# Optimization experiments

Hardware: AMD Instinct MI355X
Metric: run time of the kernel (lower is better)

## Reference

```python
import jax, jax.numpy as jnp
import numpy as np

N_NODES = 8192
GNN_DIM = 512
N_FEAT = 64
N_ITER = 4


def setup_inputs() -> dict:
    key = jax.random.key(0)
    ks = jax.random.split(key, 8)
    scale = 1.0 / np.sqrt(GNN_DIM)
    return {
        "labels": jax.random.normal(ks[0], (N_NODES, GNN_DIM), dtype=jnp.float32),
        "adj": jax.random.uniform(ks[1], (N_NODES, N_NODES), dtype=jnp.float32),
        "features": jax.random.normal(ks[2], (N_FEAT,), dtype=jnp.float32),
        "W_self": jax.random.normal(ks[3], (GNN_DIM, GNN_DIM), dtype=jnp.float32) * scale,
        "b_self": jax.random.normal(ks[4], (GNN_DIM,), dtype=jnp.float32) * scale,
        "W_neigh": jax.random.normal(ks[5], (GNN_DIM, GNN_DIM), dtype=jnp.float32) * scale,
        "W_fc": jax.random.normal(ks[6], (1, GNN_DIM + N_FEAT), dtype=jnp.float32) * scale,
        "b_fc": jax.random.normal(ks[7], (1,), dtype=jnp.float32) * scale,
    }


def reference(labels, adj, features, W_self, b_self, W_neigh, W_fc, b_fc):
    x = labels  # [N, D]
    for _ in range(N_ITER):
        acc = adj @ x                                   # [N, D] neighbor aggregation
        x = jax.nn.relu(x @ W_self.T + b_self + acc @ W_neigh.T)
    pooled = jnp.mean(x, axis=0)                        # [D]
    z = jnp.concatenate([pooled, features]) @ W_fc.T + b_fc  # [1]
    return jax.nn.sigmoid(z)
```

## Files before the change

### kernel.cpp

```cpp
#include <hip/hip_runtime.h>

typedef __bf16 bf16;
typedef bf16 bf16x8 __attribute__((ext_vector_type(8)));
typedef bf16 bf16x4 __attribute__((ext_vector_type(4)));
typedef float f32x4 __attribute__((ext_vector_type(4)));
typedef long longx2 __attribute__((ext_vector_type(2)));
typedef unsigned int u32;
typedef unsigned int u32x2 __attribute__((ext_vector_type(2)));
typedef unsigned int u32x4 __attribute__((ext_vector_type(4)));
typedef unsigned char u8;
typedef unsigned long long u64;

constexpr int NN = 8192;
constexpr int DD = 512;
constexpr size_t PSZB = (size_t)NN * DD * 2;
constexpr size_t PSZE = (size_t)NN * DD;
constexpr int NS = 4;

static __device__ inline bf16x8 cvt8(const float* __restrict__ p) {
  f32x4 a = *(const f32x4*)p;
  f32x4 b = *(const f32x4*)(p + 4);
  bf16x8 r;
  r[0] = (bf16)a[0]; r[1] = (bf16)a[1]; r[2] = (bf16)a[2]; r[3] = (bf16)a[3];
  r[4] = (bf16)b[0]; r[5] = (bf16)b[1]; r[6] = (bf16)b[2]; r[7] = (bf16)b[3];
  return r;
}

static __device__ inline unsigned f32_to_e4m3(float x) {
  float a = fabsf(x);
  unsigned s = (__float_as_uint(x) >> 24) & 0x80u;
  if (!(a < 448.f)) a = 448.f;
  if (a < 0.015625f)
    return s | (unsigned)(int)__builtin_rintf(a * 512.f);
  int e = (int)((__float_as_uint(a) >> 23) & 0xFF) - 127;
  float mul = __uint_as_float((unsigned)(130 - e) << 23);
  int t = (int)__builtin_rintf(a * mul);
  return s | (unsigned)((e + 6) * 8 + t);
}

#define GLDS(g, l) __builtin_amdgcn_global_load_lds( \
    (const __attribute__((address_space(1))) unsigned int*)(const void*)(g), \
    (__attribute__((address_space(3))) unsigned int*)(void*)(l), 16, 0, 0)


__global__ __launch_bounds__(256) void convert_w_kernel(
    const float* __restrict__ a, const float* __restrict__ b,
    bf16* __restrict__ ao, bf16* __restrict__ bo, float* __restrict__ pooled) {
  int tid = (int)threadIdx.x;
  if (blockIdx.x == 0) {
    pooled[tid] = 0.f;
    pooled[tid + 256] = 0.f;
  }
  int i8 = ((int)blockIdx.x * 256 + tid) * 8;
  if (i8 < DD * DD) {
    *(bf16x8*)&ao[i8] = cvt8(a + i8);
  } else {
    int j = i8 - DD * DD;
    *(bf16x8*)&bo[j] = cvt8(b + j);
  }
}

__global__ __launch_bounds__(256) void convert_adj_kernel(
    const float* __restrict__ a, u8* __restrict__ o) {
  int i = (int)blockIdx.x * 256 + (int)threadIdx.x;
  int row = i >> 9;
  int rem = i & 511;
  int g = rem >> 2, fq = rem & 3;
  const float* p = a + (size_t)row * NN + g * 64 + fq * 8;
  f32x4 v0 = *(const f32x4*)p;
  f32x4 v1 = *(const f32x4*)(p + 4);
  f32x4 v2 = *(const f32x4*)(p + 32);
  f32x4 v3 = *(const f32x4*)(p + 36);
  u32 w0 = 0, w1 = 0, w2 = 0, w3 = 0;
  w0 = __builtin_amdgcn_cvt_pk_fp8_f32(v0[0], v0[1], w0, false);
  w0 = __builtin_amdgcn_cvt_pk_fp8_f32(v0[2], v0[3], w0, true);
  w1 = __builtin_amdgcn_cvt_pk_fp8_f32(v1[0], v1[1], w1, false);
  w1 = __builtin_amdgcn_cvt_pk_fp8_f32(v1[2], v1[3], w1, true);
  w2 = __builtin_amdgcn_cvt_pk_fp8_f32(v2[0], v2[1], w2, false);
  w2 = __builtin_amdgcn_cvt_pk_fp8_f32(v2[2], v2[3], w2, true);
  w3 = __builtin_amdgcn_cvt_pk_fp8_f32(v3[0], v3[1], w3, false);
  w3 = __builtin_amdgcn_cvt_pk_fp8_f32(v3[2], v3[3], w3, true);
  u32x4 w; w[0] = w0; w[1] = w1; w[2] = w2; w[3] = w3;
  *(u32x4*)(o + (size_t)row * NN + g * 64 + fq * 16) = w;
}

__global__ __launch_bounds__(256) void convert_x_kernel(
    const float* __restrict__ src, bf16* __restrict__ xb, u8* __restrict__ xbT8) {
  __shared__ __align__(16) float tile[64][68];
  const int tid = (int)threadIdx.x;
  const int r0 = (int)blockIdx.x * 64;
  const int c0 = (int)blockIdx.y * 64;
#pragma unroll
  for (int p = 0; p < 4; ++p) {
    int row = p * 16 + (tid >> 4);
    int col = (tid & 15) * 4;
    *(f32x4*)&tile[row][col] = *(const f32x4*)&src[(size_t)(r0 + row) * DD + c0 + col];
  }
  __syncthreads();
#pragma unroll
  for (int p = 0; p < 4; ++p) {
    int row = p * 16 + (tid >> 4);
    int col = (tid & 15) * 4;
    f32x4 v = *(const f32x4*)&tile[row][col];
    bf16x4 o;
    o[0] = (bf16)v[0]; o[1] = (bf16)v[1]; o[2] = (bf16)v[2]; o[3] = (bf16)v[3];
    *(bf16x4*)&xb[(size_t)(r0 + row) * DD + c0 + col] = o;
  }
  {
    int c = tid >> 2;
    int rp = (tid & 3) * 16;
    size_t base = (size_t)(c0 + c) * NN + r0;
#pragma unroll
    for (int b = 0; b < 2; ++b) {
      u32 lo = 0, hi = 0;
      lo = __builtin_amdgcn_cvt_pk_fp8_f32(tile[rp + 8 * b + 0][c], tile[rp + 8 * b + 1][c], lo, false);
      lo = __builtin_amdgcn_cvt_pk_fp8_f32(tile[rp + 8 * b + 2][c], tile[rp + 8 * b + 3][c], lo, true);
      hi = __builtin_amdgcn_cvt_pk_fp8_f32(tile[rp + 8 * b + 4][c], tile[rp + 8 * b + 5][c], hi, false);
      hi = __builtin_amdgcn_cvt_pk_fp8_f32(tile[rp + 8 * b + 6][c], tile[rp + 8 * b + 7][c], hi, true);
      int u = (rp >> 3) + b;
      u32x2 w; w[0] = lo; w[1] = hi;
      *(u32x2*)&xbT8[base + (u & 3) * 16 + (u >> 2) * 8] = w;
    }
  }
}


__device__ __forceinline__ void stage_half8(const u8* __restrict__ g, int grow0, int k0b,
                                            u8* smbase, int wave, int lane) {
  int row = grow0 + wave * 16 + (lane >> 2);
  int col = k0b + (((lane & 3) ^ ((lane >> 2) & 3)) << 4);
  GLDS(g + (size_t)row * NN + col, smbase + wave * 1024);
}

__global__ __launch_bounds__(512, 2)
void gemm1_kernel(const u8* __restrict__ adjb, const u8* __restrict__ xbT8,
                  bf16* __restrict__ pbase) {
  __shared__ __align__(16) u8 sm[65536];
  const int bid  = (int)blockIdx.x;
  const int xcd  = bid & 7, ii = bid >> 3;
  const int cb   = ii & 1;
  const int jj_  = xcd + 8 * (ii >> 1);
  const int p    = jj_ >> 2;
  const int s    = jj_ & 3;
  const int prow0 = p * 256;
  const int bcol0 = cb * 256;
  const int kb    = s * 2048;
  bf16* __restrict__ P = pbase + (size_t)s * PSZE;

  const int tid  = (int)threadIdx.x;
  const int lane = tid & 63;
  const int wave = tid >> 6;
  const int wr   = wave >> 2;
  const int wc   = wave & 3;
  const int fr   = lane & 15, fq = lane >> 4;

  f32x4 acc[8][4] = {};

#define A_OFF(par) ((par) * 32768)
#define B_OFF(par) ((par) * 32768 + 16384)
#define STAGE_A(tile, half, par) \
  stage_half8(adjb, prow0 + (half) * 128, kb + ((tile) & 31) * 64, \
              sm + A_OFF(par) + (half) * 8192, wave, lane)
#define STAGE_B(tile, half, par) \
  stage_half8(xbT8, bcol0 + (half) * 128, kb + ((tile) & 31) * 64, \
              sm + B_OFF(par) + (half) * 8192, wave, lane)

  STAGE_B(0, 0, 0); STAGE_B(0, 1, 0); STAGE_A(0, 0, 0);
  STAGE_A(0, 1, 0); STAGE_B(1, 0, 1); STAGE_B(1, 1, 1); STAGE_A(1, 0, 1);

  longx2 bvp[4], afp[2];

#define LOAD_B(par)                                                        \
  _Pragma("unroll") for (int n = 0; n < 4; ++n) {                          \
    int rowl = wc * 64 + n * 16 + fr;                                      \
    int slot = fq ^ (rowl & 3);                                            \
    bvp[n] = *(const longx2*)&sm[B_OFF(par) + rowl * 64 + slot * 16];      \
  }
#define LOAD_A(q, par)                                                     \
  _Pragma("unroll") for (int j = 0; j < 2; ++j) {                          \
    int rowl = (q) * 64 + wr * 32 + j * 16 + fr;                           \
    int slot = fq ^ (rowl & 3);                                            \
    afp[j] = *(const longx2*)&sm[A_OFF(par) + rowl * 64 + slot * 16];      \
  }
#define QMFMA(q)                                                           \
  _Pragma("unroll") for (int kk = 0; kk < 2; ++kk)                         \
  _Pragma("unroll") for (int j = 0; j < 2; ++j)                            \
  _Pragma("unroll") for (int n = 0; n < 4; ++n)                            \
    acc[2 * (q) + j][n] = __builtin_amdgcn_mfma_f32_16x16x32_fp8_fp8(      \
        kk ? afp[j].y : afp[j].x, kk ? bvp[n].y : bvp[n].x,                \
        acc[2 * (q) + j][n], 0, 0, 0);
#define PHASE_TAIL(q)                                                      \
  __builtin_amdgcn_s_barrier();                                            \
  asm volatile("s_waitcnt lgkmcnt(0)" ::: "memory");                       \
  __builtin_amdgcn_sched_barrier(0);                                       \
  __builtin_amdgcn_s_setprio(1);                                           \
  QMFMA(q);                                                                \
  __builtin_amdgcn_s_setprio(0);                                           \
  __builtin_amdgcn_s_barrier();

  for (int it = 0; it < 16; ++it) {
    const int t = it * 2;
    asm volatile("s_waitcnt vmcnt(4)" ::: "memory");
    LOAD_B(0);
    LOAD_A(0, 0);
    STAGE_A(t + 1, 1, 1);
    PHASE_TAIL(0);
    LOAD_A(1, 0);
    STAGE_B(t + 2, 0, 0);
    PHASE_TAIL(1);
    asm volatile("s_waitcnt vmcnt(5)" ::: "memory");
    LOAD_A(2, 0);
    STAGE_B(t + 2, 1, 0);
    PHASE_TAIL(2);
    LOAD_A(3, 0);
    STAGE_A(t + 2, 0, 0);
    PHASE_TAIL(3);
    asm volatile("s_waitcnt vmcnt(4)" ::: "memory");
    LOAD_B(1);
    LOAD_A(0, 1);
    STAGE_A(t + 2, 1, 0);
    PHASE_TAIL(0);
    LOAD_A(1, 1);
    STAGE_B(t + 3, 0, 1);
    PHASE_TAIL(1);
    asm volatile("s_waitcnt vmcnt(5)" ::: "memory");
    LOAD_A(2, 1);
    STAGE_B(t + 3, 1, 1);
    PHASE_TAIL(2);
    LOAD_A(3, 1);
    STAGE_A(t + 3, 0, 1);
    PHASE_TAIL(3);
  }

#pragma unroll
  for (int m = 0; m < 8; ++m)
#pragma unroll
    for (int n = 0; n < 4; ++n)
#pragma unroll
      for (int r = 0; r < 4; ++r) {
        int row = prow0 + (m >> 1) * 64 + wr * 32 + (m & 1) * 16 + fq * 4 + r;
        int col = bcol0 + wc * 64 + n * 16 + fr;
        P[(size_t)row * DD + col] = (bf16)acc[m][n][r];
      }
#undef A_OFF
#undef B_OFF
#undef STAGE_A
#undef STAGE_B
#undef LOAD_B
#undef LOAD_A
#undef QMFMA
#undef PHASE_TAIL
}

__global__ __launch_bounds__(1024, 4)
void gemm2_kernel(const bf16* __restrict__ wsb, const bf16* __restrict__ wnb,
                  bf16* __restrict__ xb, const bf16* __restrict__ pbase,
                  const float* __restrict__ bself, u8* __restrict__ xbT8,
                  float* __restrict__ pooled, int dopool,
                  float alpha, float inv_an) {
  __shared__ __align__(16) char smem[139264];
  const int tid  = (int)threadIdx.x;
  const int lane = tid & 63;
  const int wave = tid >> 6;
  const int n0 = (int)blockIdx.x * 32;
  const int fr = lane & 15, fq = lane >> 4;
  const int srow = lane >> 3;
  const int scol = ((lane & 7) ^ (srow & 7)) * 8;
  const int fnode = tid >> 3, fks = tid & 7;

  f32x4 acc[2][2] = {};

  {
    bf16* la = (bf16*)smem;
#pragma unroll
    for (int c = 0; c < 4; ++c) {
      int chunk = wave * 4 + c;
      GLDS(wsb + (size_t)(chunk * 8 + srow) * DD + scol, &la[chunk * 512]);
    }
    if (wave < 4)
      GLDS(xb + (size_t)(n0 + wave * 8 + srow) * DD + scol,
           &((bf16*)(smem + 131072))[wave * 512]);
  }
  asm volatile("s_waitcnt vmcnt(0)" ::: "memory");
  __builtin_amdgcn_s_barrier();

  for (int t = 0; t < 16; ++t) {
    const int par = t & 1;
    bf16* la = (bf16*)(smem + par * 65536);
    bf16* lb = (bf16*)(smem + 131072 + par * 4096);

    bf16x8 fv0, fv1, fv2, fv3;
    bool fold = false;
    if (t < 15) {
      const int tn = t + 1, prn = tn >> 3, k0n = (tn & 7) * 64;
      const bf16* __restrict__ An = prn ? wnb : wsb;
      bf16* lan = (bf16*)(smem + (par ^ 1) * 65536);
#pragma unroll
      for (int c = 0; c < 4; ++c) {
        int chunk = wave * 4 + c;
        GLDS(An + (size_t)(chunk * 8 + srow) * DD + k0n + scol, &lan[chunk * 512]);
      }
      if (prn == 0) {
        if (wave < 4)
          GLDS(xb + (size_t)(n0 + wave * 8 + srow) * DD + k0n + scol,
               &((bf16*)(smem + 131072 + (par ^ 1) * 4096))[wave * 512]);
      } else if (tid < 256) {
        fold = true;
        const bf16* p0 = pbase + (size_t)(n0 + fnode) * DD + k0n + fks * 8;
        fv0 = *(const bf16x8*)(p0);
        fv1 = *(const bf16x8*)(p0 + PSZE);
        fv2 = *(const bf16x8*)(p0 + 2 * PSZE);
        fv3 = *(const bf16x8*)(p0 + 3 * PSZE);
      }
    }

    bf16x8 af[2][2], bv[2][2];
#pragma unroll
    for (int kk = 0; kk < 2; ++kk) {
#pragma unroll
      for (int m = 0; m < 2; ++m) {
        int rowl = wave * 32 + m * 16 + fr;
        int slot = (kk * 4 + fq) ^ (rowl & 7);
        af[kk][m] = *(const bf16x8*)&la[rowl * 64 + slot * 8];
      }
#pragma unroll
      for (int n = 0; n < 2; ++n) {
        int rowl = n * 16 + fr;
        int slot = (kk * 4 + fq) ^ (rowl & 7);
        bv[kk][n] = *(const bf16x8*)&lb[rowl * 64 + slot * 8];
      }
    }
#pragma unroll
    for (int kk = 0; kk < 2; ++kk)
#pragma unroll
      for (int m = 0; m < 2; ++m)
#pragma unroll
        for (int n = 0; n < 2; ++n)
          acc[m][n] = __builtin_amdgcn_mfma_f32_16x16x32_bf16(af[kk][m], bv[kk][n], acc[m][n], 0, 0, 0);

    if (fold) {
      bf16x8 o;
#pragma unroll
      for (int j = 0; j < 8; ++j)
        o[j] = (bf16)(((float)fv0[j] + (float)fv1[j] + (float)fv2[j] + (float)fv3[j]) * alpha);
      *(bf16x8*)&((bf16*)(smem + 131072 + (par ^ 1) * 4096))[fnode * 64 + (fks ^ (fnode & 7)) * 8] = o;
    }

    asm volatile("s_waitcnt vmcnt(0) lgkmcnt(0)" ::: "memory");
    __builtin_amdgcn_s_barrier();
  }

  bf16* lds_t = (bf16*)smem;
  u8*   lds8  = (u8*)(smem + 40960);
#pragma unroll
  for (int m = 0; m < 2; ++m)
#pragma unroll
    for (int n = 0; n < 2; ++n)
#pragma unroll
      for (int r = 0; r < 4; ++r) {
        int d = wave * 32 + m * 16 + fq * 4 + r;
        int node = n * 16 + fr;
        float v = acc[m][n][r] + bself[d];
        v = v > 0.f ? v : 0.f;
        lds_t[node * 520 + d] = (bf16)v;
        lds8[d * 32 + node] = (u8)f32_to_e4m3(v * inv_an);
      }
  if (dopool) {
#pragma unroll
    for (int m = 0; m < 2; ++m)
#pragma unroll
      for (int r = 0; r < 4; ++r) {
        int d = wave * 32 + m * 16 + fq * 4 + r;
        float b = bself[d];
        float v0 = acc[m][0][r] + b, v1 = acc[m][1][r] + b;
        float sv = (v0 > 0.f ? v0 : 0.f) + (v1 > 0.f ? v1 : 0.f);
        sv += __shfl_xor(sv, 1);
        sv += __shfl_xor(sv, 2);
        sv += __shfl_xor(sv, 4);
        sv += __shfl_xor(sv, 8);
        if (fr == 0) atomicAdd(&pooled[d], sv);
      }
  }
  __syncthreads();
  {
    int node = tid >> 5;
    int dc = (tid & 31) * 16;
    bf16x8 v0 = *(const bf16x8*)&lds_t[node * 520 + dc];
    bf16x8 v1 = *(const bf16x8*)&lds_t[node * 520 + dc + 8];
    *(bf16x8*)&xb[(size_t)(n0 + node) * DD + dc] = v0;
    *(bf16x8*)&xb[(size_t)(n0 + node) * DD + dc + 8] = v1;
  }
  {
    int d = tid >> 1, half = tid & 1;
    const u64* src = (const u64*)&lds8[d * 32 + half * 16];
    u64 w0 = src[0], w1 = src[1];
    size_t base = (size_t)d * NN + (size_t)(n0 & ~63) + ((n0 >> 5) & 1) * 8;
    *(u64*)&xbT8[base + half * 32] = w0;
    *(u64*)&xbT8[base + half * 32 + 16] = w1;
  }
}


__global__ __launch_bounds__(64) void final_kernel(
    const float* __restrict__ pooled, const float* __restrict__ features,
    const float* __restrict__ wfc, const float* __restrict__ bfc,
    float* __restrict__ out) {
  const int t = (int)threadIdx.x;
  float s = 0.f;
  for (int i = t; i < DD + 64; i += 64) {
    float v = (i < DD) ? pooled[i] * (1.0f / (float)NN) : features[i - DD];
    s += v * wfc[i];
  }
#pragma unroll
  for (int off = 32; off > 0; off >>= 1) s += __shfl_down(s, off);
  if (t == 0) {
    float z = s + bfc[0];
    out[0] = 1.0f / (1.0f + expf(-z));
  }
}


extern "C" void kernel_launch(void* const* d_in, const int* in_sizes, int n_in,
                              void* d_out, int out_size, void* d_ws, size_t ws_size,
                              hipStream_t stream) {
  const float* labels   = (const float*)d_in[0];
  const float* adj      = (const float*)d_in[1];
  const float* features = (const float*)d_in[2];
  const float* W_self   = (const float*)d_in[3];
  const float* b_self   = (const float*)d_in[4];
  const float* W_neigh  = (const float*)d_in[5];
  const float* W_fc     = (const float*)d_in[6];
  const float* b_fc     = (const float*)d_in[7];
  float* out = (float*)d_out;

  const float AL[5] = {1.f, 4.f, 2048.f, 4194304.f, 1.f};

  char* ws = (char*)d_ws;
  bf16*  xb    = (bf16*)(ws);
  u8*    xbT8  = (u8*)(ws + PSZB);
  bf16*  pbase = (bf16*)(ws + 2 * PSZB);
  char*  after_p = ws + (size_t)(2 + NS) * PSZB;
  bf16*  wsb    = (bf16*)(after_p);
  bf16*  wnb    = (bf16*)(after_p + 524288);
  float* pooled = (float*)(after_p + 1048576);
  u8*    adjb8  = (u8*)(after_p + 1048576 + 4096);

  convert_w_kernel<<<2 * DD * DD / 8 / 256, 256, 0, stream>>>(W_self, W_neigh, wsb, wnb, pooled);
  convert_adj_kernel<<<(int)((size_t)NN * NN / 16 / 256), 256, 0, stream>>>(adj, adjb8);
  convert_x_kernel<<<dim3(NN / 64, DD / 64), 256, 0, stream>>>(labels, xb, xbT8);

  for (int it = 0; it < 4; ++it) {
    gemm1_kernel<<<256, 512, 0, stream>>>(adjb8, xbT8, pbase);
    gemm2_kernel<<<NN / 32, 1024, 0, stream>>>(wsb, wnb, xb, pbase, b_self, xbT8,
                                               pooled, it == 3 ? 1 : 0,
                                               AL[it], 1.f / AL[it + 1]);
  }

  final_kernel<<<1, 64, 0, stream>>>(pooled, features, W_fc, b_fc, out);
}
```

Before: 412.4 us.

## Halve gemm1 row tile to 128, double grid, and skip final-iteration x writeback

```diff
diff --git a/kernel.cpp b/kernel.cpp
--- a/kernel.cpp
+++ b/kernel.cpp
@@ -132,17 +132,16 @@
   GLDS(g + (size_t)row * NN + col, smbase + wave * 1024);
 }
 
-__global__ __launch_bounds__(512, 2)
+__global__ __launch_bounds__(512, 4)
 void gemm1_kernel(const u8* __restrict__ adjb, const u8* __restrict__ xbT8,
                   bf16* __restrict__ pbase) {
-  __shared__ __align__(16) u8 sm[65536];
+  __shared__ __align__(16) u8 sm[49152];
   const int bid  = (int)blockIdx.x;
-  const int xcd  = bid & 7, ii = bid >> 3;
-  const int cb   = ii & 1;
-  const int jj_  = xcd + 8 * (ii >> 1);
-  const int p    = jj_ >> 2;
-  const int s    = jj_ & 3;
-  const int prow0 = p * 256;
+  const int xcd  = bid & 7;
+  const int p    = bid >> 3;
+  const int s    = xcd >> 1;
+  const int cb   = xcd & 1;
+  const int prow0 = p * 128;
   const int bcol0 = cb * 256;
   const int kb    = s * 2048;
   bf16* __restrict__ P = pbase + (size_t)s * PSZE;
@@ -154,19 +153,19 @@
   const int wc   = wave & 3;
   const int fr   = lane & 15, fq = lane >> 4;
 
-  f32x4 acc[8][4] = {};
-
-#define A_OFF(par) ((par) * 32768)
-#define B_OFF(par) ((par) * 32768 + 16384)
-#define STAGE_A(tile, half, par) \
-  stage_half8(adjb, prow0 + (half) * 128, kb + ((tile) & 31) * 64, \
-              sm + A_OFF(par) + (half) * 8192, wave, lane)
+  f32x4 acc[4][4] = {};
+
+#define A_OFF(par) ((par) * 24576)
+#define B_OFF(par) ((par) * 24576 + 8192)
+#define STAGE_A(tile, par) \
+  stage_half8(adjb, prow0, kb + ((tile) & 31) * 64, sm + A_OFF(par), wave, lane)
 #define STAGE_B(tile, half, par) \
   stage_half8(xbT8, bcol0 + (half) * 128, kb + ((tile) & 31) * 64, \
               sm + B_OFF(par) + (half) * 8192, wave, lane)
-
-  STAGE_B(0, 0, 0); STAGE_B(0, 1, 0); STAGE_A(0, 0, 0);
-  STAGE_A(0, 1, 0); STAGE_B(1, 0, 1); STAGE_B(1, 1, 1); STAGE_A(1, 0, 1);
+#define BARRIER() __builtin_amdgcn_s_barrier(); __builtin_amdgcn_sched_barrier(0)
+
+  STAGE_B(0, 0, 0); STAGE_B(0, 1, 0); STAGE_A(0, 0);
+  STAGE_B(1, 0, 1); STAGE_B(1, 1, 1);
 
   longx2 bvp[4], afp[2];
 
@@ -176,69 +175,44 @@
     int slot = fq ^ (rowl & 3);                                            \
     bvp[n] = *(const longx2*)&sm[B_OFF(par) + rowl * 64 + slot * 16];      \
   }
-#define LOAD_A(q, par)                                                     \
+#define LOAD_A2(qb, par)                                                   \
   _Pragma("unroll") for (int j = 0; j < 2; ++j) {                          \
-    int rowl = (q) * 64 + wr * 32 + j * 16 + fr;                           \
+    int rowl = wr * 64 + ((qb) + j) * 16 + fr;                             \
     int slot = fq ^ (rowl & 3);                                            \
     afp[j] = *(const longx2*)&sm[A_OFF(par) + rowl * 64 + slot * 16];      \
   }
-#define QMFMA(q)                                                           \
+#define HMFMA(qb)                                                          \
+  __builtin_amdgcn_s_setprio(1);                                           \
   _Pragma("unroll") for (int kk = 0; kk < 2; ++kk)                         \
   _Pragma("unroll") for (int j = 0; j < 2; ++j)                            \
   _Pragma("unroll") for (int n = 0; n < 4; ++n)                            \
-    acc[2 * (q) + j][n] = __builtin_amdgcn_mfma_f32_16x16x32_fp8_fp8(      \
+    acc[(qb) + j][n] = __builtin_amdgcn_mfma_f32_16x16x32_fp8_fp8(         \
         kk ? afp[j].y : afp[j].x, kk ? bvp[n].y : bvp[n].x,                \
-        acc[2 * (q) + j][n], 0, 0, 0);
-#define PHASE_TAIL(q)                                                      \
-  __builtin_amdgcn_s_barrier();                                            \
-  asm volatile("s_waitcnt lgkmcnt(0)" ::: "memory");                       \
-  __builtin_amdgcn_sched_barrier(0);                                       \
-  __builtin_amdgcn_s_setprio(1);                                           \
-  QMFMA(q);                                                                \
-  __builtin_amdgcn_s_setprio(0);                                           \
-  __builtin_amdgcn_s_barrier();
-
-  for (int it = 0; it < 16; ++it) {
-    const int t = it * 2;
-    asm volatile("s_waitcnt vmcnt(4)" ::: "memory");
-    LOAD_B(0);
-    LOAD_A(0, 0);
-    STAGE_A(t + 1, 1, 1);
-    PHASE_TAIL(0);
-    LOAD_A(1, 0);
-    STAGE_B(t + 2, 0, 0);
-    PHASE_TAIL(1);
-    asm volatile("s_waitcnt vmcnt(5)" ::: "memory");
-    LOAD_A(2, 0);
-    STAGE_B(t + 2, 1, 0);
-    PHASE_TAIL(2);
-    LOAD_A(3, 0);
-    STAGE_A(t + 2, 0, 0);
-    PHASE_TAIL(3);
-    asm volatile("s_waitcnt vmcnt(4)" ::: "memory");
-    LOAD_B(1);
-    LOAD_A(0, 1);
-    STAGE_A(t + 2, 1, 0);
-    PHASE_TAIL(0);
-    LOAD_A(1, 1);
-    STAGE_B(t + 3, 0, 1);
-    PHASE_TAIL(1);
-    asm volatile("s_waitcnt vmcnt(5)" ::: "memory");
-    LOAD_A(2, 1);
-    STAGE_B(t + 3, 1, 1);
-    PHASE_TAIL(2);
-    LOAD_A(3, 1);
-    STAGE_A(t + 3, 0, 1);
-    PHASE_TAIL(3);
-  }
-
-#pragma unroll
-  for (int m = 0; m < 8; ++m)
+        acc[(qb) + j][n], 0, 0, 0);                                        \
+  __builtin_amdgcn_s_setprio(0);
+
+  int par = 0;
+  for (int t = 0; t < 32; ++t, par ^= 1) {
+    asm volatile("s_waitcnt vmcnt(2)" ::: "memory");
+    BARRIER();
+    LOAD_B(par);
+    LOAD_A2(0, par);
+    STAGE_A(t + 1, par ^ 1);
+    HMFMA(0);
+    BARRIER();
+    LOAD_A2(2, par);
+    STAGE_B(t + 2, 0, par);
+    STAGE_B(t + 2, 1, par);
+    HMFMA(2);
+  }
+
+#pragma unroll
+  for (int m = 0; m < 4; ++m)
 #pragma unroll
     for (int n = 0; n < 4; ++n)
 #pragma unroll
       for (int r = 0; r < 4; ++r) {
-        int row = prow0 + (m >> 1) * 64 + wr * 32 + (m & 1) * 16 + fq * 4 + r;
+        int row = prow0 + wr * 64 + m * 16 + fq * 4 + r;
         int col = bcol0 + wc * 64 + n * 16 + fr;
         P[(size_t)row * DD + col] = (bf16)acc[m][n][r];
       }
@@ -247,9 +221,9 @@
 #undef STAGE_A
 #undef STAGE_B
 #undef LOAD_B
-#undef LOAD_A
-#undef QMFMA
-#undef PHASE_TAIL
+#undef LOAD_A2
+#undef HMFMA
+#undef BARRIER
 }
 
 __global__ __launch_bounds__(1024, 4)
@@ -350,21 +324,6 @@
     __builtin_amdgcn_s_barrier();
   }
 
-  bf16* lds_t = (bf16*)smem;
-  u8*   lds8  = (u8*)(smem + 40960);
-#pragma unroll
-  for (int m = 0; m < 2; ++m)
-#pragma unroll
-    for (int n = 0; n < 2; ++n)
-#pragma unroll
-      for (int r = 0; r < 4; ++r) {
-        int d = wave * 32 + m * 16 + fq * 4 + r;
-        int node = n * 16 + fr;
-        float v = acc[m][n][r] + bself[d];
-        v = v > 0.f ? v : 0.f;
-        lds_t[node * 520 + d] = (bf16)v;
-        lds8[d * 32 + node] = (u8)f32_to_e4m3(v * inv_an);
-      }
   if (dopool) {
 #pragma unroll
     for (int m = 0; m < 2; ++m)
@@ -380,7 +339,24 @@
         sv += __shfl_xor(sv, 8);
         if (fr == 0) atomicAdd(&pooled[d], sv);
       }
-  }
+    return;
+  }
+
+  bf16* lds_t = (bf16*)smem;
+  u8*   lds8  = (u8*)(smem + 40960);
+#pragma unroll
+  for (int m = 0; m < 2; ++m)
+#pragma unroll
+    for (int n = 0; n < 2; ++n)
+#pragma unroll
+      for (int r = 0; r < 4; ++r) {
+        int d = wave * 32 + m * 16 + fq * 4 + r;
+        int node = n * 16 + fr;
+        float v = acc[m][n][r] + bself[d];
+        v = v > 0.f ? v : 0.f;
+        lds_t[node * 520 + d] = (bf16)v;
+        lds8[d * 32 + node] = (u8)f32_to_e4m3(v * inv_an);
+      }
   __syncthreads();
   {
     int node = tid >> 5;
@@ -450,7 +426,7 @@
   convert_x_kernel<<<dim3(NN / 64, DD / 64), 256, 0, stream>>>(labels, xb, xbT8);
 
   for (int it = 0; it < 4; ++it) {
-    gemm1_kernel<<<256, 512, 0, stream>>>(adjb8, xbT8, pbase);
+    gemm1_kernel<<<512, 512, 0, stream>>>(adjb8, xbT8, pbase);
     gemm2_kernel<<<NN / 32, 1024, 0, stream>>>(wsb, wnb, xb, pbase, b_self, xbT8,
                                                pooled, it == 3 ? 1 : 0,
                                                AL[it], 1.f / AL[it + 1]);
```

Measured after the change: 376.6 us. 1.09x faster.
